# Kernel tuning notes

Measured on AMD Instinct MI355X. Metric: run time of the kernel, lower is better.

Reference implementation:

```python
import jax, jax.numpy as jnp
import numpy as np

WORD_EMB_DIM = 100
TAG_EMB_DIM = 28
EMB_DIM = WORD_EMB_DIM + TAG_EMB_DIM  # 128; LSTM hidden size per direction
HID = EMB_DIM
WORD_VOCAB = 50000
TAG_VOCAB = 50
B = 16
L = 128


def _lstm_dir(x, w_ih, w_hh, b_ih, b_hh, reverse):
    # x: [B, T, In] -> [B, T, H]; PyTorch gate order i, f, g, o
    xT = jnp.swapaxes(x, 0, 1)  # [T, B, In]
    if reverse:
        xT = xT[::-1]
    xp = jnp.einsum('tbi,gi->tbg', xT, w_ih) + b_ih + b_hh  # [T, B, 4H]
    H = w_hh.shape[1]

    def step(carry, g_x):
        h, c = carry
        g = g_x + h @ w_hh.T
        i, f, gg, o = jnp.split(g, 4, axis=-1)
        c = jax.nn.sigmoid(f) * c + jax.nn.sigmoid(i) * jnp.tanh(gg)
        h = jax.nn.sigmoid(o) * jnp.tanh(c)
        return (h, c), h

    h0 = jnp.zeros((x.shape[0], H), x.dtype)
    _, hs = jax.lax.scan(step, (h0, h0), xp)
    if reverse:
        hs = hs[::-1]
    return jnp.swapaxes(hs, 0, 1)


def _bilstm(x, pf, pb):
    return jnp.concatenate([_lstm_dir(x, *pf, reverse=False),
                            _lstm_dir(x, *pb, reverse=True)], axis=-1)


def setup_inputs() -> dict:
    key = jax.random.key(0)
    ks = iter(jax.random.split(key, 40))

    def rn(shape, s=0.1):
        return (jax.random.normal(next(ks), shape) * s).astype(jnp.float32)

    inp = {
        'words_idx': jax.random.randint(next(ks), (B, L), 0, WORD_VOCAB),
        'pos_idx': jax.random.randint(next(ks), (B, L), 0, TAG_VOCAB),
        'max_length': L,
        'lengths': jax.random.randint(next(ks), (B,), 1, L + 1),
        'word_emb': rn((WORD_VOCAB, WORD_EMB_DIM)),
        'tag_emb': rn((TAG_VOCAB, TAG_EMB_DIM)),
    }
    for l, insz in ((0, EMB_DIM), (1, 2 * HID)):
        for d in ('f', 'b'):
            inp[f'w_ih_l{l}{d}'] = rn((4 * HID, insz))
            inp[f'w_hh_l{l}{d}'] = rn((4 * HID, HID))
            inp[f'b_ih_l{l}{d}'] = rn((4 * HID,))
            inp[f'b_hh_l{l}{d}'] = rn((4 * HID,))
    inp['fc1_w'] = rn((100, 4 * EMB_DIM))
    inp['fc1_b'] = rn((100,))
    inp['fc2_w'] = rn((1, 100))
    inp['fc2_b'] = rn((1,))
    return inp


def reference(words_idx, pos_idx, max_length, lengths, word_emb, tag_emb,
              w_ih_l0f, w_hh_l0f, b_ih_l0f, b_hh_l0f,
              w_ih_l0b, w_hh_l0b, b_ih_l0b, b_hh_l0b,
              w_ih_l1f, w_hh_l1f, b_ih_l1f, b_hh_l1f,
              w_ih_l1b, w_hh_l1b, b_ih_l1b, b_hh_l1b,
              fc1_w, fc1_b, fc2_w, fc2_b):
    # embeddings + concat -> [B, L, EMB_DIM]
    x = jnp.concatenate([word_emb[words_idx[:, :max_length]],
                         tag_emb[pos_idx[:, :max_length]]], axis=-1)
    h = _bilstm(x, (w_ih_l0f, w_hh_l0f, b_ih_l0f, b_hh_l0f),
                (w_ih_l0b, w_hh_l0b, b_ih_l0b, b_hh_l0b))
    h = _bilstm(h, (w_ih_l1f, w_hh_l1f, b_ih_l1f, b_hh_l1f),
                (w_ih_l1b, w_hh_l1b, b_ih_l1b, b_hh_l1b))  # [B, L, 2*HID]
    # Pairwise feature(i,j) = cat(h[:,i], h[:,j]); fuse fc1 by splitting its
    # weight into head/dependent halves -> broadcast-add instead of L^2 concat.
    D = h.shape[-1]
    wa, wb = fc1_w[:, :D], fc1_w[:, D:]
    a = jnp.einsum('bld,kd->blk', h, wa)                 # [B, L, 100]
    bp = jnp.einsum('bld,kd->blk', h, wb) + fc1_b        # [B, L, 100]
    hid = jnp.tanh(a[:, :, None, :] + bp[:, None, :, :])  # [B, L, L, 100]
    scores = jnp.einsum('bijk,ok->bijo', hid, fc2_w) + fc2_b  # [B, L, L, 1]
    # original stacks features along axis 0 in (i outer, j inner) order
    return scores.transpose(1, 2, 0, 3).reshape(max_length * max_length, -1, 1)
```

## Files before the change

### kernel.cpp

```cpp
#include <hip/hip_runtime.h>

typedef float v2f __attribute__((ext_vector_type(2)));

__device__ __forceinline__ float frcp(float x){ return __builtin_amdgcn_rcpf(x); }
__device__ __forceinline__ float fexp2(float x){ return __builtin_amdgcn_exp2f(x); }
__device__ __forceinline__ float sigf(float x){ return frcp(1.f + fexp2(-1.4426950408889634f*x)); }
__device__ __forceinline__ float tanh_(float x){ return 1.f - 2.f*frcp(1.f + fexp2(2.8853900817779268f*x)); }

__global__ __launch_bounds__(256) void embed_kernel(
    const int* __restrict__ widx, const int* __restrict__ pidx,
    const float* __restrict__ wemb, const float* __restrict__ temb,
    float* __restrict__ x)
{
    int gid = blockIdx.x*256 + threadIdx.x;
    int bt = gid >> 7, c = gid & 127;
    float v;
    if (c < 100) v = wemb[(size_t)widx[bt]*100 + c];
    else         v = temb[(size_t)pidx[bt]*28 + (c-100)];
    x[gid] = v;
}

__global__ __launch_bounds__(256) void gemm_kernel(
    const float* __restrict__ A, int K,
    const float* __restrict__ B0, const float* __restrict__ B1, int ldb,
    const float* __restrict__ bias0a, const float* __restrict__ bias0b,
    const float* __restrict__ bias1a, const float* __restrict__ bias1b,
    float* __restrict__ C0, float* __restrict__ C1, int ldc, int N,
    int expflag, int permflag)
{
    __shared__ float As[16][140];
    __shared__ float Bs[16][68];
    const int z = blockIdx.z;
    const float* B  = z ? B1 : B0;
    const float* ba = z ? bias1a : bias0a;
    const float* bb = z ? bias1b : bias0b;
    float* C = z ? C1 : C0;
    const int m0 = blockIdx.x * 128;
    const int n0 = blockIdx.y * 64;
    const int tx = threadIdx.x;
    const int tm = tx & 15, tn = tx >> 4;
    const int arow = tx >> 1, akq = (tx & 1) * 8;
    const int brow = tx >> 2, bkq = (tx & 3) * 4;
    const int g_arow = arow + 4*(arow >> 5);
    const int rbase = tm*8 + 4*(tm >> 2);
    float acc[8][4];
    #pragma unroll
    for (int r=0;r<8;++r){
        #pragma unroll
        for (int c=0;c<4;++c) acc[r][c]=0.f; }
    const int bn = n0 + brow;
    const int brow_src = permflag ? ((bn & 3)*128 + (bn >> 2)) : bn;
    for (int k0 = 0; k0 < K; k0 += 16) {
        const float* ap = A + (size_t)(m0+arow)*K + k0 + akq;
        float4 a0 = *(const float4*)ap;
        float4 a1 = *(const float4*)(ap+4);
        float4 bv = make_float4(0.f,0.f,0.f,0.f);
        if (bn < N) {
            const float* bp = B + (size_t)brow_src*ldb + k0 + bkq;
            bv = *(const float4*)bp;
        }
        __syncthreads();
        As[akq+0][g_arow]=a0.x; As[akq+1][g_arow]=a0.y; As[akq+2][g_arow]=a0.z; As[akq+3][g_arow]=a0.w;
        As[akq+4][g_arow]=a1.x; As[akq+5][g_arow]=a1.y; As[akq+6][g_arow]=a1.z; As[akq+7][g_arow]=a1.w;
        Bs[bkq+0][brow]=bv.x; Bs[bkq+1][brow]=bv.y; Bs[bkq+2][brow]=bv.z; Bs[bkq+3][brow]=bv.w;
        __syncthreads();
        #pragma unroll
        for (int kk = 0; kk < 16; ++kk) {
            float4 av0 = *(const float4*)&As[kk][rbase];
            float4 av1 = *(const float4*)&As[kk][rbase+4];
            float4 bvv = *(const float4*)&Bs[kk][tn*4];
            float a[8] = {av0.x,av0.y,av0.z,av0.w,av1.x,av1.y,av1.z,av1.w};
            float b[4] = {bvv.x,bvv.y,bvv.z,bvv.w};
            #pragma unroll
            for (int r=0;r<8;++r){
                #pragma unroll
                for (int c=0;c<4;++c)
                    acc[r][c] = fmaf(a[r], b[c], acc[r][c]);
            }
        }
    }
    float bias[4];
    #pragma unroll
    for (int c=0;c<4;++c) {
        int n = n0 + tn*4 + c;
        int nsrc = permflag ? ((n & 3)*128 + (n >> 2)) : n;
        float v = 0.f;
        if (n < N) {
            if (ba) v += ba[nsrc];
            if (bb) v += bb[nsrc];
        }
        bias[c] = v;
    }
    #pragma unroll
    for (int r=0;r<8;++r) {
        int m = m0 + tm*8 + r;
        float v[4];
        #pragma unroll
        for (int c=0;c<4;++c) {
            float t = acc[r][c] + bias[c];
            if (expflag) t = fexp2(fminf(fmaxf(t,-40.f),40.f)*2.8853900817779268f);
            v[c] = t;
        }
        int n = n0 + tn*4;
        if (n + 3 < N) {
            float4 st; st.x=v[0]; st.y=v[1]; st.z=v[2]; st.w=v[3];
            *(float4*)&C[(size_t)m*ldc + n] = st;
        } else {
            #pragma unroll
            for (int c=0;c<4;++c) if (n+c < N) C[(size_t)m*ldc + n + c] = v[c];
        }
    }
}

__global__ __launch_bounds__(512, 2)
void lstm_kernel(
    const float* __restrict__ xp,
    const float* whh_f, const float* whh_b,
    float* hcat)
{
    const int b = blockIdx.x & 15;
    const int dir = blockIdx.x >> 4;
    const int t = threadIdx.x;
    const int q  = t & 3;
    const int gc = (t >> 2) & 3;
    const int rp = t >> 4;
    const float* whh = dir ? whh_b : whh_f;
    const int G = (gc == 0) ? 0 : (gc == 1) ? 2 : (gc == 2) ? 1 : 3;
    const float kexp = (gc == 1) ? 2.8853900817779268f : -1.4426950408889634f;
    const float mA   = (gc == 1) ? -2.f : 1.f;
    const float mB   = (gc == 1) ?  1.f : 0.f;

    v2f wA[32], wB[32];
    {
        const float* wr = whh + (size_t)(G*128 + 4*rp)*128 + 32*q;
        #pragma unroll
        for (int j = 0; j < 32; j += 4) {
            float4 r0 = *(const float4*)(wr + j);
            float4 r1 = *(const float4*)(wr + 128 + j);
            float4 r2 = *(const float4*)(wr + 256 + j);
            float4 r3 = *(const float4*)(wr + 384 + j);
            wA[j+0] = (v2f){r0.x, r1.x}; wB[j+0] = (v2f){r2.x, r3.x};
            wA[j+1] = (v2f){r0.y, r1.y}; wB[j+1] = (v2f){r2.y, r3.y};
            wA[j+2] = (v2f){r0.z, r1.z}; wB[j+2] = (v2f){r2.z, r3.z};
            wA[j+3] = (v2f){r0.w, r1.w}; wB[j+3] = (v2f){r2.w, r3.w};
        }
    }

    __shared__ float h_lds[2][140];
    float c = 0.f;
    if (t < 128) h_lds[0][t + 4*(t >> 5)] = 0.f;
    __syncthreads();

    const float* xpd = xp + (size_t)dir*(2048*512) + (size_t)b*(128*512);
    const int myrow = 4*rp + q;
    const int mycol = 4*myrow + G;
    const int mystore = myrow + 4*(myrow >> 5);
    float xpv = xpd[(dir ? 127 : 0)*512 + mycol];

    for (int s = 0; s < 128; ++s) {
        const int ts = dir ? (127 - s) : s;
        const int tsn = dir ? (126 - s < 0 ? 0 : 126 - s) : (s + 1 > 127 ? 127 : s + 1);
        float xnext = xpd[tsn*512 + mycol];
        const float* hb = &h_lds[s & 1][36*q];
        v2f aA = (v2f){0.f,0.f}, aB = (v2f){0.f,0.f};
        #pragma unroll
        for (int j = 0; j < 32; j += 4) {
            float4 h4 = *(const float4*)&hb[j];
            aA += wA[j+0] * (v2f){h4.x, h4.x};  aB += wB[j+0] * (v2f){h4.x, h4.x};
            aA += wA[j+1] * (v2f){h4.y, h4.y};  aB += wB[j+1] * (v2f){h4.y, h4.y};
            aA += wA[j+2] * (v2f){h4.z, h4.z};  aB += wB[j+2] * (v2f){h4.z, h4.z};
            aA += wA[j+3] * (v2f){h4.w, h4.w};  aB += wB[j+3] * (v2f){h4.w, h4.w};
        }
        float a0 = aA.x, a1 = aA.y, a2 = aB.x, a3 = aB.y;
        a0 += __shfl_xor(a0, 1, 64); a1 += __shfl_xor(a1, 1, 64);
        a2 += __shfl_xor(a2, 1, 64); a3 += __shfl_xor(a3, 1, 64);
        a0 += __shfl_xor(a0, 2, 64); a1 += __shfl_xor(a1, 2, 64);
        a2 += __shfl_xor(a2, 2, 64); a3 += __shfl_xor(a3, 2, 64);
        float dsel = (q & 2) ? ((q & 1) ? a3 : a2) : ((q & 1) ? a1 : a0);
        float dot = xpv + dsel;
        float act = fmaf(mA, frcp(1.f + fexp2(kexp*dot)), mB);
        float o1 = __uint_as_float(__builtin_amdgcn_ds_swizzle(__float_as_uint(act), 0x101F));
        float v1 = (gc < 2) ? act * o1 : ((gc == 2) ? act : o1);
        float o2 = __uint_as_float(__builtin_amdgcn_ds_swizzle(__float_as_uint(v1), 0x201F));
        float Af = (gc < 2) ? o2 : ((gc == 2) ? act : o1);
        float Bf = (gc < 2) ? v1 : o2;
        c = fmaf(Af, c, Bf);
        float th = tanh_(c);
        float sigo = (gc == 2) ? o1 : act;
        float h = sigo * th;
        if (gc == 2) {
            h_lds[(s & 1) ^ 1][mystore] = h;
            hcat[((size_t)b*128 + ts)*256 + dir*128 + myrow] = h;
        }
        xpv = xnext;
        __syncthreads();
    }
}

__global__ __launch_bounds__(256) void pair_kernel(
    const float* __restrict__ ea, const float* __restrict__ eb,
    const float* __restrict__ fc2w, const float* __restrict__ fc2b,
    float* __restrict__ out)
{
    __shared__ float eas[32][100];
    __shared__ float ebs[32][100];
    __shared__ float w2s[100];
    __shared__ float red[128];
    const int it = blockIdx.x * 32, jt = blockIdx.y * 32, b = blockIdx.z;
    const int tx = threadIdx.x;
    const float* eab = ea + (size_t)b*12800;
    const float* ebb = eb + (size_t)b*12800;
    for (int idx = tx; idx < 3200; idx += 256) {
        int r = idx / 100;
        int cc = idx - r*100;
        eas[r][cc] = eab[(it + r)*100 + cc];
        ebs[r][cc] = ebb[(jt + r)*100 + cc];
    }
    if (tx < 128) {
        float wv = (tx < 100) ? fc2w[tx] : 0.f;
        if (tx < 100) w2s[tx] = -2.f*wv;
        red[tx] = wv;
    }
    __syncthreads();
    for (int s2 = 64; s2 > 0; s2 >>= 1) {
        if (tx < s2) red[tx] += red[tx+s2];
        __syncthreads();
    }
    const float S = red[0] + fc2b[0];
    const int jp = tx & 15, ip = tx >> 4;
    const int i0 = ip*2, j0 = jp*2;
    float acc00=S, acc01=S, acc10=S, acc11=S;
    #pragma unroll
    for (int k = 0; k < 100; k += 4) {
        float4 A0 = *(const float4*)&eas[i0][k];
        float4 A1 = *(const float4*)&eas[i0+1][k];
        float4 B0 = *(const float4*)&ebs[j0][k];
        float4 B1 = *(const float4*)&ebs[j0+1][k];
        float4 W  = *(const float4*)&w2s[k];
        acc00 = fmaf(W.x, frcp(fmaf(A0.x,B0.x,1.f)), acc00);
        acc01 = fmaf(W.x, frcp(fmaf(A0.x,B1.x,1.f)), acc01);
        acc10 = fmaf(W.x, frcp(fmaf(A1.x,B0.x,1.f)), acc10);
        acc11 = fmaf(W.x, frcp(fmaf(A1.x,B1.x,1.f)), acc11);
        acc00 = fmaf(W.y, frcp(fmaf(A0.y,B0.y,1.f)), acc00);
        acc01 = fmaf(W.y, frcp(fmaf(A0.y,B1.y,1.f)), acc01);
        acc10 = fmaf(W.y, frcp(fmaf(A1.y,B0.y,1.f)), acc10);
        acc11 = fmaf(W.y, frcp(fmaf(A1.y,B1.y,1.f)), acc11);
        acc00 = fmaf(W.z, frcp(fmaf(A0.z,B0.z,1.f)), acc00);
        acc01 = fmaf(W.z, frcp(fmaf(A0.z,B1.z,1.f)), acc01);
        acc10 = fmaf(W.z, frcp(fmaf(A1.z,B0.z,1.f)), acc10);
        acc11 = fmaf(W.z, frcp(fmaf(A1.z,B1.z,1.f)), acc11);
        acc00 = fmaf(W.w, frcp(fmaf(A0.w,B0.w,1.f)), acc00);
        acc01 = fmaf(W.w, frcp(fmaf(A0.w,B1.w,1.f)), acc01);
        acc10 = fmaf(W.w, frcp(fmaf(A1.w,B0.w,1.f)), acc10);
        acc11 = fmaf(W.w, frcp(fmaf(A1.w,B1.w,1.f)), acc11);
    }
    const int gi0 = it + i0, gj0 = jt + j0;
    out[((size_t)(gi0  )*128 + gj0  )*16 + b] = acc00;
    out[((size_t)(gi0  )*128 + gj0+1)*16 + b] = acc01;
    out[((size_t)(gi0+1)*128 + gj0  )*16 + b] = acc10;
    out[((size_t)(gi0+1)*128 + gj0+1)*16 + b] = acc11;
}

extern "C" void kernel_launch(void* const* d_in, const int* in_sizes, int n_in,
                              void* d_out, int out_size, void* d_ws, size_t ws_size,
                              hipStream_t stream)
{
    (void)in_sizes; (void)n_in; (void)out_size; (void)ws_size;
    const int*   widx = (const int*)d_in[0];
    const int*   pidx = (const int*)d_in[1];
    const float* wemb = (const float*)d_in[4];
    const float* temb = (const float*)d_in[5];
    const float* w_ih_l0f = (const float*)d_in[6];
    const float* w_hh_l0f = (const float*)d_in[7];
    const float* b_ih_l0f = (const float*)d_in[8];
    const float* b_hh_l0f = (const float*)d_in[9];
    const float* w_ih_l0b = (const float*)d_in[10];
    const float* w_hh_l0b = (const float*)d_in[11];
    const float* b_ih_l0b = (const float*)d_in[12];
    const float* b_hh_l0b = (const float*)d_in[13];
    const float* w_ih_l1f = (const float*)d_in[14];
    const float* w_hh_l1f = (const float*)d_in[15];
    const float* b_ih_l1f = (const float*)d_in[16];
    const float* b_hh_l1f = (const float*)d_in[17];
    const float* w_ih_l1b = (const float*)d_in[18];
    const float* w_hh_l1b = (const float*)d_in[19];
    const float* b_ih_l1b = (const float*)d_in[20];
    const float* b_hh_l1b = (const float*)d_in[21];
    const float* fc1_w = (const float*)d_in[22];
    const float* fc1_b = (const float*)d_in[23];
    const float* fc2_w = (const float*)d_in[24];
    const float* fc2_b = (const float*)d_in[25];

    float* ws  = (float*)d_ws;
    float* x   = ws;
    float* xp0 = x + 262144;
    float* h1  = xp0 + 2097152;
    float* xp1 = h1 + 524288;
    float* h2  = xp1 + 2097152;
    float* ea  = h2 + 524288;
    float* eb  = ea + 204800;

    embed_kernel<<<1024, 256, 0, stream>>>(widx, pidx, wemb, temb, x);
    gemm_kernel<<<dim3(16,8,2), 256, 0, stream>>>(x, 128,
        w_ih_l0f, w_ih_l0b, 128,
        b_ih_l0f, b_hh_l0f, b_ih_l0b, b_hh_l0b,
        xp0, xp0 + 1048576, 512, 512, 0, 1);
    lstm_kernel<<<32, 512, 0, stream>>>(xp0, w_hh_l0f, w_hh_l0b, h1);
    gemm_kernel<<<dim3(16,8,2), 256, 0, stream>>>(h1, 256,
        w_ih_l1f, w_ih_l1b, 256,
        b_ih_l1f, b_hh_l1f, b_ih_l1b, b_hh_l1b,
        xp1, xp1 + 1048576, 512, 512, 0, 1);
    lstm_kernel<<<32, 512, 0, stream>>>(xp1, w_hh_l1f, w_hh_l1b, h2);
    gemm_kernel<<<dim3(16,2,2), 256, 0, stream>>>(h2, 256,
        fc1_w, fc1_w + 256, 512,
        nullptr, nullptr, fc1_b, nullptr,
        ea, eb, 100, 100, 1, 0);
    pair_kernel<<<dim3(4,4,16), 256, 0, stream>>>(ea, eb, fc2_w, fc2_b, (float*)d_out);
}
```

Before: 392.9 us.

## Use packed fp16 recurrent weights with fdot2 in LSTM kernel

Adds a pack kernel that converts the recurrent weight matrices to fp16 pairs in a per-thread layout. The LSTM step now computes its gate dot products with fdot2 against an fp16 copy of the hidden state. One quarter of each thread's weights is staged in LDS and the rest stays in registers. This halves weight storage and the FMA count on the serial recurrence critical path. The cost is reduced precision in h and W_hh, plus one extra kernel launch.

Measured after the change: 390.3 us. No clear change (-0.6%).

```diff
diff --git a/kernel.cpp b/kernel.cpp
--- a/kernel.cpp
+++ b/kernel.cpp
@@ -1,11 +1,24 @@
 #include <hip/hip_runtime.h>
 
-typedef float v2f __attribute__((ext_vector_type(2)));
+typedef _Float16 h2 __attribute__((ext_vector_type(2)));
 
 __device__ __forceinline__ float frcp(float x){ return __builtin_amdgcn_rcpf(x); }
 __device__ __forceinline__ float fexp2(float x){ return __builtin_amdgcn_exp2f(x); }
-__device__ __forceinline__ float sigf(float x){ return frcp(1.f + fexp2(-1.4426950408889634f*x)); }
 __device__ __forceinline__ float tanh_(float x){ return 1.f - 2.f*frcp(1.f + fexp2(2.8853900817779268f*x)); }
+
+#if __has_builtin(__builtin_amdgcn_fdot2)
+#define FDOT2(a,b,c) __builtin_amdgcn_fdot2((a),(b),(c),false)
+#else
+#define FDOT2(a,b,c) ((c) + (float)(a).x*(float)(b).x + (float)(a).y*(float)(b).y)
+#endif
+
+__device__ __forceinline__ float dotu4(uint4 wv, uint4 hv, float acc){
+    acc = FDOT2(__builtin_bit_cast(h2, wv.x), __builtin_bit_cast(h2, hv.x), acc);
+    acc = FDOT2(__builtin_bit_cast(h2, wv.y), __builtin_bit_cast(h2, hv.y), acc);
+    acc = FDOT2(__builtin_bit_cast(h2, wv.z), __builtin_bit_cast(h2, hv.z), acc);
+    acc = FDOT2(__builtin_bit_cast(h2, wv.w), __builtin_bit_cast(h2, hv.w), acc);
+    return acc;
+}
 
 __global__ __launch_bounds__(256) void embed_kernel(
     const int* __restrict__ widx, const int* __restrict__ pidx,
@@ -18,6 +31,24 @@
     if (c < 100) v = wemb[(size_t)widx[bt]*100 + c];
     else         v = temb[(size_t)pidx[bt]*28 + (c-100)];
     x[gid] = v;
+}
+
+__global__ __launch_bounds__(256) void pack_kernel(
+    const float* __restrict__ w0f, const float* __restrict__ w0b,
+    const float* __restrict__ w1f, const float* __restrict__ w1b,
+    unsigned* __restrict__ wpk0, unsigned* __restrict__ wpk1)
+{
+    int id = blockIdx.x*256 + threadIdx.x;
+    int L = id >> 16, d = (id >> 15) & 1, t = (id >> 6) & 511, j = id & 63;
+    const float* whh = L ? (d ? w1b : w1f) : (d ? w0b : w0f);
+    unsigned* dst = L ? wpk1 : wpk0;
+    int q = t & 3, gc = (t >> 2) & 3, rp = t >> 4;
+    int G = (gc == 0) ? 0 : (gc == 1) ? 2 : (gc == 2) ? 1 : 3;
+    int row = j >> 4, kp = j & 15;
+    const float* src = whh + (size_t)(G*128 + 4*rp + row)*128 + 32*q + 2*kp;
+    unsigned short a = __builtin_bit_cast(unsigned short, (_Float16)src[0]);
+    unsigned short b = __builtin_bit_cast(unsigned short, (_Float16)src[1]);
+    dst[((size_t)d*512 + t)*64 + j] = (unsigned)a | ((unsigned)b << 16);
 }
 
 __global__ __launch_bounds__(256) void gemm_kernel(
@@ -115,7 +146,7 @@
 __global__ __launch_bounds__(512, 2)
 void lstm_kernel(
     const float* __restrict__ xp,
-    const float* whh_f, const float* whh_b,
+    const unsigned* wpk,
     float* hcat)
 {
     const int b = blockIdx.x & 15;
@@ -124,59 +155,60 @@
     const int q  = t & 3;
     const int gc = (t >> 2) & 3;
     const int rp = t >> 4;
-    const float* whh = dir ? whh_b : whh_f;
+    const int wave = t >> 6, lane = t & 63;
     const int G = (gc == 0) ? 0 : (gc == 1) ? 2 : (gc == 2) ? 1 : 3;
     const float kexp = (gc == 1) ? 2.8853900817779268f : -1.4426950408889634f;
     const float mA   = (gc == 1) ? -2.f : 1.f;
     const float mB   = (gc == 1) ?  1.f : 0.f;
 
-    v2f wA[32], wB[32];
+    __shared__ uint4 wlds4[2048];
+    __shared__ _Float16 h_lds[2][128];
+
+    const unsigned* wr = wpk + ((size_t)dir*512 + t)*64;
     {
-        const float* wr = whh + (size_t)(G*128 + 4*rp)*128 + 32*q;
-        #pragma unroll
-        for (int j = 0; j < 32; j += 4) {
-            float4 r0 = *(const float4*)(wr + j);
-            float4 r1 = *(const float4*)(wr + 128 + j);
-            float4 r2 = *(const float4*)(wr + 256 + j);
-            float4 r3 = *(const float4*)(wr + 384 + j);
-            wA[j+0] = (v2f){r0.x, r1.x}; wB[j+0] = (v2f){r2.x, r3.x};
-            wA[j+1] = (v2f){r0.y, r1.y}; wB[j+1] = (v2f){r2.y, r3.y};
-            wA[j+2] = (v2f){r0.z, r1.z}; wB[j+2] = (v2f){r2.z, r3.z};
-            wA[j+3] = (v2f){r0.w, r1.w}; wB[j+3] = (v2f){r2.w, r3.w};
-        }
-    }
-
-    __shared__ float h_lds[2][140];
+        #pragma unroll
+        for (int i = 0; i < 4; ++i)
+            wlds4[(wave*4 + i)*64 + lane] = *(const uint4*)(wr + 4*i);
+    }
+    uint4 u1[4], u2[4], u3[4];
+    #pragma unroll
+    for (int i = 0; i < 4; ++i) {
+        u1[i] = *(const uint4*)(wr + 16 + 4*i);
+        u2[i] = *(const uint4*)(wr + 32 + 4*i);
+        u3[i] = *(const uint4*)(wr + 48 + 4*i);
+    }
+
     float c = 0.f;
-    if (t < 128) h_lds[0][t + 4*(t >> 5)] = 0.f;
+    if (t < 128) h_lds[0][t] = (_Float16)0.f;
     __syncthreads();
 
     const float* xpd = xp + (size_t)dir*(2048*512) + (size_t)b*(128*512);
     const int myrow = 4*rp + q;
     const int mycol = 4*myrow + G;
-    const int mystore = myrow + 4*(myrow >> 5);
     float xpv = xpd[(dir ? 127 : 0)*512 + mycol];
 
     for (int s = 0; s < 128; ++s) {
         const int ts = dir ? (127 - s) : s;
         const int tsn = dir ? (126 - s < 0 ? 0 : 126 - s) : (s + 1 > 127 ? 127 : s + 1);
         float xnext = xpd[tsn*512 + mycol];
-        const float* hb = &h_lds[s & 1][36*q];
-        v2f aA = (v2f){0.f,0.f}, aB = (v2f){0.f,0.f};
-        #pragma unroll
-        for (int j = 0; j < 32; j += 4) {
-            float4 h4 = *(const float4*)&hb[j];
-            aA += wA[j+0] * (v2f){h4.x, h4.x};  aB += wB[j+0] * (v2f){h4.x, h4.x};
-            aA += wA[j+1] * (v2f){h4.y, h4.y};  aB += wB[j+1] * (v2f){h4.y, h4.y};
-            aA += wA[j+2] * (v2f){h4.z, h4.z};  aB += wB[j+2] * (v2f){h4.z, h4.z};
-            aA += wA[j+3] * (v2f){h4.w, h4.w};  aB += wB[j+3] * (v2f){h4.w, h4.w};
-        }
-        float a0 = aA.x, a1 = aA.y, a2 = aB.x, a3 = aB.y;
-        a0 += __shfl_xor(a0, 1, 64); a1 += __shfl_xor(a1, 1, 64);
-        a2 += __shfl_xor(a2, 1, 64); a3 += __shfl_xor(a3, 1, 64);
-        a0 += __shfl_xor(a0, 2, 64); a1 += __shfl_xor(a1, 2, 64);
-        a2 += __shfl_xor(a2, 2, 64); a3 += __shfl_xor(a3, 2, 64);
-        float dsel = (q & 2) ? ((q & 1) ? a3 : a2) : ((q & 1) ? a1 : a0);
+        const uint4* hb = (const uint4*)&h_lds[s & 1][0];
+        uint4 hv[4];
+        #pragma unroll
+        for (int i = 0; i < 4; ++i) hv[i] = hb[q*4 + i];
+        float d0 = 0.f, d1 = 0.f, d2 = 0.f, d3 = 0.f;
+        #pragma unroll
+        for (int i = 0; i < 4; ++i) {
+            uint4 wl = wlds4[(wave*4 + i)*64 + lane];
+            d0 = dotu4(wl,    hv[i], d0);
+            d1 = dotu4(u1[i], hv[i], d1);
+            d2 = dotu4(u2[i], hv[i], d2);
+            d3 = dotu4(u3[i], hv[i], d3);
+        }
+        d0 += __shfl_xor(d0, 1, 64); d1 += __shfl_xor(d1, 1, 64);
+        d2 += __shfl_xor(d2, 1, 64); d3 += __shfl_xor(d3, 1, 64);
+        d0 += __shfl_xor(d0, 2, 64); d1 += __shfl_xor(d1, 2, 64);
+        d2 += __shfl_xor(d2, 2, 64); d3 += __shfl_xor(d3, 2, 64);
+        float dsel = (q & 2) ? ((q & 1) ? d3 : d2) : ((q & 1) ? d1 : d0);
         float dot = xpv + dsel;
         float act = fmaf(mA, frcp(1.f + fexp2(kexp*dot)), mB);
         float o1 = __uint_as_float(__builtin_amdgcn_ds_swizzle(__float_as_uint(act), 0x101F));
@@ -189,7 +221,7 @@
         float sigo = (gc == 2) ? o1 : act;
         float h = sigo * th;
         if (gc == 2) {
-            h_lds[(s & 1) ^ 1][mystore] = h;
+            h_lds[(s & 1) ^ 1][myrow] = (_Float16)h;
             hcat[((size_t)b*128 + ts)*256 + dir*128 + myrow] = h;
         }
         xpv = xnext;
@@ -299,18 +331,21 @@
     float* h2  = xp1 + 2097152;
     float* ea  = h2 + 524288;
     float* eb  = ea + 204800;
+    unsigned* wpk0 = (unsigned*)(eb + 204800);
+    unsigned* wpk1 = wpk0 + 65536;
 
     embed_kernel<<<1024, 256, 0, stream>>>(widx, pidx, wemb, temb, x);
+    pack_kernel<<<512, 256, 0, stream>>>(w_hh_l0f, w_hh_l0b, w_hh_l1f, w_hh_l1b, wpk0, wpk1);
     gemm_kernel<<<dim3(16,8,2), 256, 0, stream>>>(x, 128,
         w_ih_l0f, w_ih_l0b, 128,
         b_ih_l0f, b_hh_l0f, b_ih_l0b, b_hh_l0b,
         xp0, xp0 + 1048576, 512, 512, 0, 1);
-    lstm_kernel<<<32, 512, 0, stream>>>(xp0, w_hh_l0f, w_hh_l0b, h1);
+    lstm_kernel<<<32, 512, 0, stream>>>(xp0, wpk0, h1);
     gemm_kernel<<<dim3(16,8,2), 256, 0, stream>>>(h1, 256,
         w_ih_l1f, w_ih_l1b, 256,
         b_ih_l1f, b_hh_l1f, b_ih_l1b, b_hh_l1b,
         xp1, xp1 + 1048576, 512, 512, 0, 1);
-    lstm_kernel<<<32, 512, 0, stream>>>(xp1, w_hh_l1f, w_hh_l1b, h2);
+    lstm_kernel<<<32, 512, 0, stream>>>(xp1, wpk1, h2);
     gemm_kernel<<<dim3(16,2,2), 256, 0, stream>>>(h2, 256,
         fc1_w, fc1_w + 256, 512,
         nullptr, nullptr, fc1_b, nullptr,
```
